# Optimization experiments

Measured on AMD Instinct MI355X. Metric: run time of the kernel, lower is better.

## Reference

```python
import jax, jax.numpy as jnp
import numpy as np

HID, NH, HD, KTS = 512, 8, 64, 4
BATCH, SEQ = 2, 1024
CLIP, AMIN, AMAX = 2.0, 1e-4, 0.9995
ROPE_BASE = 10000.0


def _rmsnorm(x, w, eps=1e-5):
    rms = jnp.sqrt(jnp.mean(x * x, axis=-1, keepdims=True) + eps)
    return x / rms * w


def _rope(q, k, base=ROPE_BASE):
    # q,k: [B,T,H,D], D even -> rotate-half formulation (split halves, not interleaved)
    T, D = q.shape[1], q.shape[-1]
    half = D // 2
    pos = jnp.arange(T, dtype=q.dtype)
    inv_freq = 1.0 / (base ** (jnp.arange(half, dtype=q.dtype) / half))
    ang = pos[:, None] * inv_freq[None, :]            # [T, half]
    cos = jnp.cos(ang)[None, :, None, :]
    sin = jnp.sin(ang)[None, :, None, :]
    def rot(x):
        x1, x2 = x[..., :half], x[..., half:]
        return jnp.concatenate([x1 * cos - x2 * sin, x1 * sin + x2 * cos], axis=-1)
    return rot(q), rot(k)


def setup_inputs() -> dict:
    key = jax.random.key(0)
    ks = jax.random.split(key, 10)
    def xavier(k, shape):
        lim = float(np.sqrt(6.0 / (shape[0] + shape[1])))
        return jax.random.uniform(k, shape, jnp.float32, -lim, lim)
    x = jax.random.normal(ks[0], (BATCH, SEQ, HID), jnp.float32)
    mask = jnp.ones((BATCH, SEQ), jnp.int32)
    qW = xavier(ks[1], (HID, HID))
    kW = xavier(ks[2], (HID, HID))
    vW = xavier(ks[3], (HID, HID))
    oW = xavier(ks[4], (HID, HID))
    ob = jnp.zeros((HID,), jnp.float32)
    # alpha bias from geometric half-lives [32,128,512,2048]
    half_lives = np.array([32.0 * (4.0 ** i) for i in range(KTS)], dtype=np.float64)
    alphas = np.clip(np.exp(-np.log(2.0) / half_lives), AMIN, AMAX)
    alphas = np.tile(alphas, NH)
    ab = jnp.asarray(np.log(alphas / (1.0 - alphas)), jnp.float32)
    aW = 0.01 * jax.random.normal(ks[5], (NH * KTS, HID), jnp.float32)
    mW = 0.01 * jax.random.normal(ks[6], (NH * KTS, HID), jnp.float32)
    mb = jnp.zeros((NH * KTS,), jnp.float32)
    in_w = jnp.ones((HID,), jnp.float32)
    kn_w = jnp.ones((HD,), jnp.float32)
    vn_w = jnp.ones((HD,), jnp.float32)
    ln_w = jnp.ones((HID,), jnp.float32)
    ln_b = jnp.zeros((HID,), jnp.float32)
    return dict(x=x, in_w=in_w, qW=qW, kW=kW, vW=vW, aW=aW, ab=ab, mW=mW, mb=mb,
                oW=oW, ob=ob, kn_w=kn_w, vn_w=vn_w, ln_w=ln_w, ln_b=ln_b, mask=mask)


def reference(x, in_w, qW, kW, vW, aW, ab, mW, mb, oW, ob, kn_w, vn_w, ln_w, ln_b, mask):
    B, T, _ = x.shape
    xn = _rmsnorm(x, in_w)
    q = (xn @ qW.T).reshape(B, T, NH, HD)
    k = (xn @ kW.T).reshape(B, T, NH, HD)
    v = (xn @ vW.T).reshape(B, T, NH, HD)
    q, k = _rope(q, k)
    k = _rmsnorm(k, kn_w)
    v = _rmsnorm(v, vn_w)
    alpha = jnp.clip(jax.nn.sigmoid(xn @ aW.T + ab), AMIN, AMAX).reshape(B, T, NH, KTS)
    mix = jax.nn.softmax((xn @ mW.T + mb).reshape(B, T, NH, KTS), axis=-1)
    m = mask.astype(jnp.float32)
    c = float(np.sqrt(HD)) * CLIP

    def step(h, inp):
        # h: [B,H,K,D,D] fp32 state; delta-rule write + multi-timescale decay + norm clip
        q_t, k_t, v_t, a_t, mx_t, m_t = inp
        outer = (k_t * m_t[:, None, None])[:, :, None, :, None] * v_t[:, :, None, None, :]
        h = h * a_t[..., None, None] + outer
        norm = jnp.sqrt(jnp.sum(h * h, axis=(-2, -1), keepdims=True))
        h = h * jnp.minimum(c / (norm + 1e-6), 1.0)
        y = jnp.einsum('bhd,bhkde->bhke', q_t, h)
        return h, jnp.einsum('bhk,bhkd->bhd', mx_t, y)

    h0 = jnp.zeros((B, NH, KTS, HD, HD), jnp.float32)
    tm = lambda a: jnp.moveaxis(a, 1, 0)  # time-major
    xs = (tm(q), tm(k), tm(v), tm(alpha), tm(mix), m.T)
    _, ys = jax.lax.scan(jax.checkpoint(step), h0, xs)  # ys: [T,B,H,D]
    y = jnp.moveaxis(ys, 0, 1).reshape(B, T, HID)
    out = y @ oW.T + ob  # dropout p=0 (eval)
    r = x + out
    mu = jnp.mean(r, axis=-1, keepdims=True)
    var = jnp.mean((r - mu) ** 2, axis=-1, keepdims=True)
    return (r - mu) / jnp.sqrt(var + 1e-5) * ln_w + ln_b
```

## Files before the change

### kernel.cpp

```cpp
#include <hip/hip_runtime.h>
#include <math.h>

#define SEQT 1024
#define NTOK 2048
#define HIDN 512
#define NHD 8
#define HDIM 64
#define KTSN 4

__device__ __forceinline__ float wred(float v) {
#pragma unroll
  for (int off = 32; off; off >>= 1) v += __shfl_xor(v, off, 64);
  return v;
}

template <int CTRL>
__device__ __forceinline__ float rra(float v) {
  return v + __int_as_float(__builtin_amdgcn_update_dpp(
                 0, __float_as_int(v), CTRL, 0xf, 0xf, true));
}
__device__ __forceinline__ float rlane(float v, int l) {
  return __int_as_float(__builtin_amdgcn_readlane(__float_as_int(v), l));
}
__device__ __forceinline__ float wsum64_fast(float v) {
  v = rra<0x121>(v);
  v = rra<0x122>(v);
  v = rra<0x124>(v);
  v = rra<0x128>(v);
  return (rlane(v, 0) + rlane(v, 16)) + (rlane(v, 32) + rlane(v, 48));
}

__global__ __launch_bounds__(256) void k_rmsnorm_in(
    const float* __restrict__ x, const float* __restrict__ w, float* __restrict__ xn) {
  int m = blockIdx.x;
  int tid = threadIdx.x;
  const float* row = x + (size_t)m * HIDN;
  float2 v = *(const float2*)(row + tid * 2);
  float ss = wred(v.x * v.x + v.y * v.y);
  __shared__ float red[4];
  int lane = tid & 63, wv = tid >> 6;
  if (lane == 0) red[wv] = ss;
  __syncthreads();
  float tot = red[0] + red[1] + red[2] + red[3];
  float inv = rsqrtf(tot * (1.0f / HIDN) + 1e-5f);
  float2 wv2 = *(const float2*)(w + tid * 2);
  float2 o;
  o.x = v.x * inv * wv2.x;
  o.y = v.y * inv * wv2.y;
  *(float2*)(xn + (size_t)m * HIDN + tid * 2) = o;
}

__global__ __launch_bounds__(256) void k_gemm_qkv(
    const float* __restrict__ A, const float* __restrict__ Bq,
    const float* __restrict__ Bk, const float* __restrict__ Bv,
    float* __restrict__ Cq, float* __restrict__ Ck, float* __restrict__ Cv) {
  __shared__ __align__(16) float As[32][68];
  __shared__ __align__(16) float Bs0[32][68];
  __shared__ __align__(16) float Bs1[32][68];
  __shared__ __align__(16) float Bs2[32][68];
  int tid = threadIdx.x;
  int m0 = blockIdx.x * 64, n0 = blockIdx.y * 64;
  int tm = tid >> 4, tn = tid & 15;
  float aq[4][4] = {}, ak[4][4] = {}, av4[4][4] = {};
  int rr = tid >> 2, cc = (tid & 3) * 8;
  for (int k0 = 0; k0 < HIDN; k0 += 32) {
    const float* s0 = A + (size_t)(m0 + rr) * HIDN + k0 + cc;
    float4 a0 = *(const float4*)s0;
    float4 a1 = *(const float4*)(s0 + 4);
    As[cc + 0][rr] = a0.x; As[cc + 1][rr] = a0.y; As[cc + 2][rr] = a0.z; As[cc + 3][rr] = a0.w;
    As[cc + 4][rr] = a1.x; As[cc + 5][rr] = a1.y; As[cc + 6][rr] = a1.z; As[cc + 7][rr] = a1.w;
    size_t boff = (size_t)(n0 + rr) * HIDN + k0 + cc;
    float4 b0 = *(const float4*)(Bq + boff);
    float4 b1 = *(const float4*)(Bq + boff + 4);
    Bs0[cc + 0][rr] = b0.x; Bs0[cc + 1][rr] = b0.y; Bs0[cc + 2][rr] = b0.z; Bs0[cc + 3][rr] = b0.w;
    Bs0[cc + 4][rr] = b1.x; Bs0[cc + 5][rr] = b1.y; Bs0[cc + 6][rr] = b1.z; Bs0[cc + 7][rr] = b1.w;
    b0 = *(const float4*)(Bk + boff);
    b1 = *(const float4*)(Bk + boff + 4);
    Bs1[cc + 0][rr] = b0.x; Bs1[cc + 1][rr] = b0.y; Bs1[cc + 2][rr] = b0.z; Bs1[cc + 3][rr] = b0.w;
    Bs1[cc + 4][rr] = b1.x; Bs1[cc + 5][rr] = b1.y; Bs1[cc + 6][rr] = b1.z; Bs1[cc + 7][rr] = b1.w;
    b0 = *(const float4*)(Bv + boff);
    b1 = *(const float4*)(Bv + boff + 4);
    Bs2[cc + 0][rr] = b0.x; Bs2[cc + 1][rr] = b0.y; Bs2[cc + 2][rr] = b0.z; Bs2[cc + 3][rr] = b0.w;
    Bs2[cc + 4][rr] = b1.x; Bs2[cc + 5][rr] = b1.y; Bs2[cc + 6][rr] = b1.z; Bs2[cc + 7][rr] = b1.w;
    __syncthreads();
#pragma unroll
    for (int kk = 0; kk < 32; ++kk) {
      float4 a4 = *(const float4*)&As[kk][tm * 4];
      float4 q4 = *(const float4*)&Bs0[kk][tn * 4];
      float4 k4 = *(const float4*)&Bs1[kk][tn * 4];
      float4 v4 = *(const float4*)&Bs2[kk][tn * 4];
      float aa[4] = {a4.x, a4.y, a4.z, a4.w};
      float qq[4] = {q4.x, q4.y, q4.z, q4.w};
      float kk_[4] = {k4.x, k4.y, k4.z, k4.w};
      float vv[4] = {v4.x, v4.y, v4.z, v4.w};
#pragma unroll
      for (int i = 0; i < 4; ++i)
#pragma unroll
        for (int j = 0; j < 4; ++j) {
          aq[i][j] = fmaf(aa[i], qq[j], aq[i][j]);
          ak[i][j] = fmaf(aa[i], kk_[j], ak[i][j]);
          av4[i][j] = fmaf(aa[i], vv[j], av4[i][j]);
        }
    }
    __syncthreads();
  }
#pragma unroll
  for (int i = 0; i < 4; ++i) {
    size_t mr = (size_t)(m0 + tm * 4 + i) * HIDN;
#pragma unroll
    for (int j = 0; j < 4; ++j) {
      int nc = n0 + tn * 4 + j;
      Cq[mr + nc] = aq[i][j];
      Ck[mr + nc] = ak[i][j];
      Cv[mr + nc] = av4[i][j];
    }
  }
}

__global__ __launch_bounds__(256) void k_gemm_am(
    const float* __restrict__ A, const float* __restrict__ Ba,
    const float* __restrict__ Bm, float* __restrict__ Ca, float* __restrict__ Cm) {
  __shared__ __align__(16) float As[32][68];
  __shared__ __align__(16) float Bs[32][68];
  int tid = threadIdx.x;
  int m0 = blockIdx.x * 64;
  int tm = tid >> 4, tn = tid & 15;
  float acc[4][4] = {};
  int rr = tid >> 2, cc = (tid & 3) * 8;
  for (int k0 = 0; k0 < HIDN; k0 += 32) {
    const float* s0 = A + (size_t)(m0 + rr) * HIDN + k0 + cc;
    float4 a0 = *(const float4*)s0;
    float4 a1 = *(const float4*)(s0 + 4);
    As[cc + 0][rr] = a0.x; As[cc + 1][rr] = a0.y; As[cc + 2][rr] = a0.z; As[cc + 3][rr] = a0.w;
    As[cc + 4][rr] = a1.x; As[cc + 5][rr] = a1.y; As[cc + 6][rr] = a1.z; As[cc + 7][rr] = a1.w;
    const float* s1 = ((rr < 32) ? (Ba + (size_t)rr * HIDN) : (Bm + (size_t)(rr - 32) * HIDN)) + k0 + cc;
    float4 b0 = *(const float4*)s1;
    float4 b1 = *(const float4*)(s1 + 4);
    Bs[cc + 0][rr] = b0.x; Bs[cc + 1][rr] = b0.y; Bs[cc + 2][rr] = b0.z; Bs[cc + 3][rr] = b0.w;
    Bs[cc + 4][rr] = b1.x; Bs[cc + 5][rr] = b1.y; Bs[cc + 6][rr] = b1.z; Bs[cc + 7][rr] = b1.w;
    __syncthreads();
#pragma unroll
    for (int kk = 0; kk < 32; ++kk) {
      float4 a4 = *(const float4*)&As[kk][tm * 4];
      float4 b4 = *(const float4*)&Bs[kk][tn * 4];
      float aa[4] = {a4.x, a4.y, a4.z, a4.w};
      float bb[4] = {b4.x, b4.y, b4.z, b4.w};
#pragma unroll
      for (int i = 0; i < 4; ++i)
#pragma unroll
        for (int j = 0; j < 4; ++j) acc[i][j] = fmaf(aa[i], bb[j], acc[i][j]);
    }
    __syncthreads();
  }
#pragma unroll
  for (int i = 0; i < 4; ++i) {
    int mr = m0 + tm * 4 + i;
#pragma unroll
    for (int j = 0; j < 4; ++j) {
      int nc = tn * 4 + j;
      if (nc < 32)
        Ca[(size_t)mr * 32 + nc] = acc[i][j];
      else
        Cm[(size_t)mr * 32 + nc - 32] = acc[i][j];
    }
  }
}

__global__ __launch_bounds__(256) void k_rope_table(float2* __restrict__ tab) {
  int idx = blockIdx.x * 256 + threadIdx.x;
  int t = idx >> 5, j = idx & 31;
  float invf = (float)exp2(-(double)j * (13.287712379549449 / 32.0));
  float ang = (float)t * invf;
  double s, c;
  sincos((double)ang, &s, &c);
  tab[idx] = make_float2((float)c, (float)s);
}

__global__ __launch_bounds__(256) void k_postproc(
    const float* __restrict__ q_in, const float* __restrict__ k_in, const float* __restrict__ v_in,
    const float* __restrict__ a_pre, const float* __restrict__ m_pre,
    const float* __restrict__ ab, const float* __restrict__ mb,
    const float* __restrict__ kn_w, const float* __restrict__ vn_w,
    const float2* __restrict__ tab,
    float* __restrict__ qh, float* __restrict__ kh, float* __restrict__ vh,
    float* __restrict__ av, float* __restrict__ mv) {
  int wid = blockIdx.x * 4 + (threadIdx.x >> 6);
  int lane = threadIdx.x & 63;
  int b = wid >> 13;
  int rem = wid & 8191;
  int t = rem >> 3;
  int h = rem & 7;
  size_t src = (size_t)(b * SEQT + t) * HIDN + h * HDIM + lane;
  float qv = q_in[src], kv = k_in[src], vv = v_in[src];
  float2 cs = tab[t * 32 + (lane & 31)];
  float qpart = __shfl_xor(qv, 32, 64);
  float kpart = __shfl_xor(kv, 32, 64);
  float qr = (lane < 32) ? (qv * cs.x - qpart * cs.y) : (qpart * cs.y + qv * cs.x);
  float kr = (lane < 32) ? (kv * cs.x - kpart * cs.y) : (kpart * cs.y + kv * cs.x);
  float kss = wred(kr * kr);
  float kn = kr * rsqrtf(kss * (1.0f / HDIM) + 1e-5f) * kn_w[lane];
  float vss = wred(vv * vv);
  float vn = vv * rsqrtf(vss * (1.0f / HDIM) + 1e-5f) * vn_w[lane];
  size_t dst = ((size_t)(b * NHD + h) * SEQT + t) * HDIM + lane;
  qh[dst] = qr;
  kh[dst] = kn;
  vh[dst] = vn;
  if (lane < 4) {
    int col = h * 4 + lane;
    float pa = a_pre[(size_t)(b * SEQT + t) * 32 + col] + ab[col];
    float al = 1.0f / (1.0f + expf(-pa));
    al = fminf(fmaxf(al, 1e-4f), 0.9995f);
    float pm = m_pre[(size_t)(b * SEQT + t) * 32 + col] + mb[col];
    float mx = pm;
    mx = fmaxf(mx, __shfl_xor(mx, 1, 64));
    mx = fmaxf(mx, __shfl_xor(mx, 2, 64));
    float e = expf(pm - mx);
    float sum = e;
    sum += __shfl_xor(sum, 1, 64);
    sum += __shfl_xor(sum, 2, 64);
    size_t adst = ((size_t)(b * NHD + h) * KTSN + lane) * SEQT + t;
    av[adst] = al;
    mv[adst] = e / sum;
  }
}

#define G16P(X) \
  X(0, 0) X(1, 1) X(2, 2) X(3, 3) X(4, 0) X(5, 1) X(6, 2) X(7, 3) \
  X(8, 0) X(9, 1) X(10, 2) X(11, 3) X(12, 0) X(13, 1) X(14, 2) X(15, 3)

#define DECLH(g, a) float h##g = 0.f;

#define UPDH(g, a)                                \
  {                                               \
    float ks = rlane(kqs0, g);                    \
    h##g = fmaf(h##g, ag, ks * vem);              \
    sq##a = fmaf(h##g, h##g, sq##a);              \
  }

#define YUPH(g, a)                                \
  {                                               \
    float qs = rlane(kqs0, 16 + (g));             \
    y##a = fmaf(qs, h##g, y##a);                  \
  }

__global__ __launch_bounds__(256, 1) void k_scan(
    const float* __restrict__ qh, const float* __restrict__ kh, const float* __restrict__ vh,
    const float* __restrict__ av, const float* __restrict__ mv, const int* __restrict__ mask,
    float* __restrict__ y0p, float* __restrict__ y1p, float* __restrict__ y2p,
    float* __restrict__ y3p) {
  int c = blockIdx.x;
  int kt = c & 3;
  int bh = c >> 2;
  int b = bh >> 3;
  int h = bh & 7;
  int tid = threadIdx.x;
  int w = tid >> 6;
  int lane = tid & 63;
  int dbase = w * 16;

  const float* kp = kh + (size_t)bh * SEQT * HDIM;
  const float* qp = qh + (size_t)bh * SEQT * HDIM;
  const float* vp = vh + (size_t)bh * SEQT * HDIM;
  const float* ap = av + (size_t)c * SEQT;
  const float* mp = mv + (size_t)c * SEQT;
  const int* mk = mask + (size_t)b * SEQT;
  float* ysel = (kt == 0) ? y0p : (kt == 1) ? y1p : (kt == 2) ? y2p : y3p;
  float* ypo = ysel + (size_t)(b * SEQT) * HIDN + h * HDIM + lane;

  __shared__ __align__(16) float sqb[2][4];
  __shared__ __align__(16) float ypart[2][4][64];
  __shared__ int cnt;

  G16P(DECLH)
  float gprev = 1.0f;

  int off = lane & 15;
  const float* kqbase = ((lane >> 4) & 1) ? qp : kp;
  int kqidx = dbase + off;

  float kqs0 = kqbase[kqidx];
  float kqs1 = kqbase[(size_t)1 * HDIM + kqidx];
  float kqs2 = kqbase[(size_t)2 * HDIM + kqidx];
  float vC = vp[lane], vD = vp[HDIM + lane], vE = vp[2 * HDIM + lane];
  float aC = ap[0], aD = ap[1], aE = ap[2];
  float mxC = mp[0], mxD = mp[1], mxE = mp[2];
  float mC = (float)mk[0], mD = (float)mk[1], mE = (float)mk[2];

  if (tid == 0) cnt = 0;
  __syncthreads();

  for (int t = 0; t < SEQT; ++t) {
    int t3 = t + 3;
    if (t3 > SEQT - 1) t3 = SEQT - 1;
    float kqN = kqbase[(size_t)t3 * HDIM + kqidx];
    float vN = vp[(size_t)t3 * HDIM + lane];
    float aN = ap[t3];
    float mxN = mp[t3];
    float mN = (float)mk[t3];

    float ag = aC * gprev;
    float vem = vC * mC;
    float sq0 = 0.f, sq1 = 0.f, sq2 = 0.f, sq3 = 0.f;
    G16P(UPDH)
    float sqw = wsum64_fast((sq0 + sq1) + (sq2 + sq3));
    int P = t & 1;
    if (lane == 0) sqb[P][w] = sqw;
    float y0 = 0.f, y1 = 0.f, y2 = 0.f, y3 = 0.f;
    G16P(YUPH)
    ypart[P][w][lane] = (y0 + y1) + (y2 + y3);
    asm volatile("s_waitcnt lgkmcnt(0)" ::: "memory");
    if (lane == 0) atomicAdd(&cnt, 1);
    {
      int target = 4 * (t + 1);
      while (*(volatile int*)&cnt < target) {
      }
    }
    asm volatile("" ::: "memory");
    float4 sq4 = *(const float4*)&sqb[P][0];
    float sqt = (sq4.x + sq4.y) + (sq4.z + sq4.w);
    float g = fminf(16.0f * rsqrtf(sqt), 1.0f);
    if (w == 0) {
      float ys = (ypart[P][0][lane] + ypart[P][1][lane]) +
                 (ypart[P][2][lane] + ypart[P][3][lane]);
      ypo[(size_t)t * HIDN] = (mxC * g) * ys;
    }
    gprev = g;

    kqs0 = kqs1; kqs1 = kqs2; kqs2 = kqN;
    vC = vD; vD = vE; vE = vN;
    aC = aD; aD = aE; aE = aN;
    mxC = mxD; mxD = mxE; mxE = mxN;
    mC = mD; mD = mE; mE = mN;
  }
}

__global__ __launch_bounds__(256) void k_gemm_out(
    const float* __restrict__ y0, const float* __restrict__ y1,
    const float* __restrict__ y2, const float* __restrict__ y3,
    const float* __restrict__ oW, const float* __restrict__ ob,
    const float* __restrict__ x, float* __restrict__ r) {
  __shared__ __align__(16) float As[32][68];
  __shared__ __align__(16) float Bs[32][68];
  int tid = threadIdx.x;
  int m0 = blockIdx.x * 64, n0 = blockIdx.y * 64;
  int tm = tid >> 4, tn = tid & 15;
  float acc[4][4] = {};
  int rr = tid >> 2, cc = (tid & 3) * 8;
  for (int k0 = 0; k0 < HIDN; k0 += 32) {
    size_t aoff = (size_t)(m0 + rr) * HIDN + k0 + cc;
#pragma unroll
    for (int half = 0; half < 2; ++half) {
      size_t sh = aoff + half * 4;
      float4 p0 = *(const float4*)(y0 + sh);
      float4 p1 = *(const float4*)(y1 + sh);
      float4 p2 = *(const float4*)(y2 + sh);
      float4 p3 = *(const float4*)(y3 + sh);
      int cbase = cc + half * 4;
      As[cbase + 0][rr] = p0.x + p1.x + p2.x + p3.x;
      As[cbase + 1][rr] = p0.y + p1.y + p2.y + p3.y;
      As[cbase + 2][rr] = p0.z + p1.z + p2.z + p3.z;
      As[cbase + 3][rr] = p0.w + p1.w + p2.w + p3.w;
    }
    const float* s1 = oW + (size_t)(n0 + rr) * HIDN + k0 + cc;
    float4 b0 = *(const float4*)s1;
    float4 b1 = *(const float4*)(s1 + 4);
    Bs[cc + 0][rr] = b0.x; Bs[cc + 1][rr] = b0.y; Bs[cc + 2][rr] = b0.z; Bs[cc + 3][rr] = b0.w;
    Bs[cc + 4][rr] = b1.x; Bs[cc + 5][rr] = b1.y; Bs[cc + 6][rr] = b1.z; Bs[cc + 7][rr] = b1.w;
    __syncthreads();
#pragma unroll
    for (int kk = 0; kk < 32; ++kk) {
      float4 a4 = *(const float4*)&As[kk][tm * 4];
      float4 b4 = *(const float4*)&Bs[kk][tn * 4];
      float aa[4] = {a4.x, a4.y, a4.z, a4.w};
      float bb[4] = {b4.x, b4.y, b4.z, b4.w};
#pragma unroll
      for (int i = 0; i < 4; ++i)
#pragma unroll
        for (int j = 0; j < 4; ++j) acc[i][j] += aa[i] * bb[j];
    }
    __syncthreads();
  }
#pragma unroll
  for (int i = 0; i < 4; ++i) {
    int mr = m0 + tm * 4 + i;
#pragma unroll
    for (int j = 0; j < 4; ++j) {
      int nc = n0 + tn * 4 + j;
      r[(size_t)mr * HIDN + nc] = x[(size_t)mr * HIDN + nc] + acc[i][j] + ob[nc];
    }
  }
}

__global__ __launch_bounds__(256) void k_layernorm(
    const float* __restrict__ r, const float* __restrict__ w, const float* __restrict__ bb,
    float* __restrict__ out) {
  int m = blockIdx.x;
  int tid = threadIdx.x;
  const float* row = r + (size_t)m * HIDN;
  float2 v = *(const float2*)(row + tid * 2);
  float s = wred(v.x + v.y);
  float ss = wred(v.x * v.x + v.y * v.y);
  __shared__ float r1[4], r2[4];
  int lane = tid & 63, wv = tid >> 6;
  if (lane == 0) {
    r1[wv] = s;
    r2[wv] = ss;
  }
  __syncthreads();
  float S = r1[0] + r1[1] + r1[2] + r1[3];
  float SS = r2[0] + r2[1] + r2[2] + r2[3];
  float mu = S * (1.0f / HIDN);
  float var = SS * (1.0f / HIDN) - mu * mu;
  float inv = rsqrtf(var + 1e-5f);
  float2 w2 = *(const float2*)(w + tid * 2);
  float2 b2 = *(const float2*)(bb + tid * 2);
  float2 o;
  o.x = (v.x - mu) * inv * w2.x + b2.x;
  o.y = (v.y - mu) * inv * w2.y + b2.y;
  *(float2*)(out + (size_t)m * HIDN + tid * 2) = o;
}

extern "C" void kernel_launch(void* const* d_in, const int* in_sizes, int n_in,
                              void* d_out, int out_size, void* d_ws, size_t ws_size,
                              hipStream_t stream) {
  const float* x = (const float*)d_in[0];
  const float* in_w = (const float*)d_in[1];
  const float* qW = (const float*)d_in[2];
  const float* kW = (const float*)d_in[3];
  const float* vW = (const float*)d_in[4];
  const float* aW = (const float*)d_in[5];
  const float* ab = (const float*)d_in[6];
  const float* mW = (const float*)d_in[7];
  const float* mb = (const float*)d_in[8];
  const float* oW = (const float*)d_in[9];
  const float* ob = (const float*)d_in[10];
  const float* kn_w = (const float*)d_in[11];
  const float* vn_w = (const float*)d_in[12];
  const float* ln_w = (const float*)d_in[13];
  const float* ln_b = (const float*)d_in[14];
  const int* mask = (const int*)d_in[15];

  float* ws = (float*)d_ws;
  float* xn = ws + 0;
  float* qb = ws + 1048576;
  float* kb = ws + 2097152;
  float* vb = ws + 3145728;
  float* apre = ws + 4194304;
  float* mpre = ws + 4259840;
  float2* tab = (float2*)(ws + 4325376);
  float* qh = ws + 4390912;
  float* kh = ws + 5439488;
  float* vh = ws + 6488064;
  float* avv = ws + 7536640;
  float* mvv = ws + 7602176;
  float* y3 = ws + 7667712;
  float* y0 = qb;
  float* y1 = kb;
  float* y2 = vb;
  float* rr = xn;

  k_rope_table<<<128, 256, 0, stream>>>(tab);
  k_rmsnorm_in<<<NTOK, 256, 0, stream>>>(x, in_w, xn);
  dim3 gBig(32, 8);
  k_gemm_qkv<<<gBig, 256, 0, stream>>>(xn, qW, kW, vW, qb, kb, vb);
  k_gemm_am<<<32, 256, 0, stream>>>(xn, aW, mW, apre, mpre);
  k_postproc<<<4096, 256, 0, stream>>>(qb, kb, vb, apre, mpre, ab, mb, kn_w, vn_w, tab,
                                       qh, kh, vh, avv, mvv);
  k_scan<<<64, 256, 0, stream>>>(qh, kh, vh, avv, mvv, mask, y0, y1, y2, y3);
  k_gemm_out<<<gBig, 256, 0, stream>>>(y0, y1, y2, y3, oW, ob, x, rr);
  k_layernorm<<<NTOK, 256, 0, stream>>>(rr, ln_w, ln_b, (float*)d_out);
  (void)in_sizes; (void)n_in; (void)out_size; (void)ws_size;
}
```

Before: 707.1 us.

## Scan two timesteps per barrier using algebraic norm and output recurrences

Rewrites the sequential delta-rule scan to process two timesteps per cross-wave barrier. The squared Frobenius norm and outputs are now obtained algebraically from the previous norm, h·k·v contractions and precomputed per-step scalars (q·k, |k|²|v|², adjacent-step k·k, v·v, q·k dot products). A new k_cross kernel and extra reductions in postproc produce those scalars. This halves the number of spin-barrier synchronisations on the serial critical path. In exchange it adds a kernel launch, reuses the xn workspace region for the scalar buffers, and may accumulate floating-point error in the recursive norm, which is clamped at zero.

```diff
diff --git a/kernel.cpp b/kernel.cpp
--- a/kernel.cpp
+++ b/kernel.cpp
@@ -183,7 +183,8 @@
     const float* __restrict__ kn_w, const float* __restrict__ vn_w,
     const float2* __restrict__ tab,
     float* __restrict__ qh, float* __restrict__ kh, float* __restrict__ vh,
-    float* __restrict__ av, float* __restrict__ mv) {
+    float* __restrict__ av, float* __restrict__ mv,
+    float* __restrict__ qkd, float* __restrict__ kvq) {
   int wid = blockIdx.x * 4 + (threadIdx.x >> 6);
   int lane = threadIdx.x & 63;
   int b = wid >> 13;
@@ -205,6 +206,14 @@
   qh[dst] = qr;
   kh[dst] = kn;
   vh[dst] = vn;
+  float knss = wred(kn * kn);
+  float vnss = wred(vn * vn);
+  float qkdot = wred(qr * kn);
+  if (lane == 0) {
+    size_t sdst = (size_t)(b * NHD + h) * SEQT + t;
+    qkd[sdst] = qkdot;
+    kvq[sdst] = knss * vnss;
+  }
   if (lane < 4) {
     int col = h * 4 + lane;
     float pa = a_pre[(size_t)(b * SEQT + t) * 32 + col] + ab[col];
@@ -224,28 +233,54 @@
   }
 }
 
+__global__ __launch_bounds__(256) void k_cross(
+    const float* __restrict__ qh, const float* __restrict__ kh, const float* __restrict__ vh,
+    float* __restrict__ kkx, float* __restrict__ vvx, float* __restrict__ qxx) {
+  int wid = blockIdx.x * 4 + (threadIdx.x >> 6);
+  int lane = threadIdx.x & 63;
+  int bh = wid >> 10;
+  int t = wid & 1023;
+  size_t sidx = (size_t)bh * SEQT + t;
+  if (t == 0) {
+    if (lane == 0) { kkx[sidx] = 0.f; vvx[sidx] = 0.f; qxx[sidx] = 0.f; }
+    return;
+  }
+  size_t base = (size_t)bh * SEQT * HDIM;
+  float kc = kh[base + (size_t)t * HDIM + lane];
+  float kp = kh[base + (size_t)(t - 1) * HDIM + lane];
+  float vc = vh[base + (size_t)t * HDIM + lane];
+  float vpv = vh[base + (size_t)(t - 1) * HDIM + lane];
+  float qc = qh[base + (size_t)t * HDIM + lane];
+  float s1 = wred(kc * kp);
+  float s2 = wred(vc * vpv);
+  float s3 = wred(qc * kp);
+  if (lane == 0) { kkx[sidx] = s1; vvx[sidx] = s2; qxx[sidx] = s3; }
+}
+
 #define G16P(X) \
   X(0, 0) X(1, 1) X(2, 2) X(3, 3) X(4, 0) X(5, 1) X(6, 2) X(7, 3) \
   X(8, 0) X(9, 1) X(10, 2) X(11, 3) X(12, 0) X(13, 1) X(14, 2) X(15, 3)
 
 #define DECLH(g, a) float h##g = 0.f;
-
-#define UPDH(g, a)                                \
-  {                                               \
-    float ks = rlane(kqs0, g);                    \
-    h##g = fmaf(h##g, ag, ks * vem);              \
-    sq##a = fmaf(h##g, h##g, sq##a);              \
-  }
-
-#define YUPH(g, a)                                \
-  {                                               \
-    float qs = rlane(kqs0, 16 + (g));             \
-    y##a = fmaf(qs, h##g, y##a);                  \
+#define HUP0(g, a) h##g = fmaf(h##g, ag0, rlane(kqj0, (g)) * vm0);
+#define HUP1(g, a) h##g = fmaf(h##g, ag1, rlane(kqj1, (g)) * vm1);
+#define MV4(g, a)                                   \
+  {                                                 \
+    float k2_ = rlane(kqj2, (g));                   \
+    float q2_ = rlane(kqj2, 16 + (g));              \
+    float k3_ = rlane(kqj3, (g));                   \
+    float q3_ = rlane(kqj3, 16 + (g));              \
+    zk2##a = fmaf(k2_, h##g, zk2##a);               \
+    zk3##a = fmaf(k3_, h##g, zk3##a);               \
+    pv2##a = fmaf(q2_, h##g, pv2##a);               \
+    pv3##a = fmaf(q3_, h##g, pv3##a);               \
   }
 
 __global__ __launch_bounds__(256, 1) void k_scan(
     const float* __restrict__ qh, const float* __restrict__ kh, const float* __restrict__ vh,
     const float* __restrict__ av, const float* __restrict__ mv, const int* __restrict__ mask,
+    const float* __restrict__ qkd, const float* __restrict__ kvq,
+    const float* __restrict__ kkx, const float* __restrict__ vvx, const float* __restrict__ qxx,
     float* __restrict__ y0p, float* __restrict__ y1p, float* __restrict__ y2p,
     float* __restrict__ y3p) {
   int c = blockIdx.x;
@@ -263,74 +298,134 @@
   const float* vp = vh + (size_t)bh * SEQT * HDIM;
   const float* ap = av + (size_t)c * SEQT;
   const float* mp = mv + (size_t)c * SEQT;
+  const float* qkp = qkd + (size_t)bh * SEQT;
+  const float* kvp = kvq + (size_t)bh * SEQT;
+  const float* kkp = kkx + (size_t)bh * SEQT;
+  const float* vvp = vvx + (size_t)bh * SEQT;
+  const float* qxp = qxx + (size_t)bh * SEQT;
   const int* mk = mask + (size_t)b * SEQT;
   float* ysel = (kt == 0) ? y0p : (kt == 1) ? y1p : (kt == 2) ? y2p : y3p;
   float* ypo = ysel + (size_t)(b * SEQT) * HIDN + h * HDIM + lane;
 
-  __shared__ __align__(16) float sqb[2][4];
-  __shared__ __align__(16) float ypart[2][4][64];
+  __shared__ __align__(16) float2 Zb[2][4];
+  __shared__ __align__(16) float Pb[2][2][4][64];
   __shared__ int cnt;
 
   G16P(DECLH)
   float gprev = 1.0f;
+  float usq = 0.0f;
 
   int off = lane & 15;
   const float* kqbase = ((lane >> 4) & 1) ? qp : kp;
   int kqidx = dbase + off;
 
-  float kqs0 = kqbase[kqidx];
-  float kqs1 = kqbase[(size_t)1 * HDIM + kqidx];
-  float kqs2 = kqbase[(size_t)2 * HDIM + kqidx];
-  float vC = vp[lane], vD = vp[HDIM + lane], vE = vp[2 * HDIM + lane];
-  float aC = ap[0], aD = ap[1], aE = ap[2];
-  float mxC = mp[0], mxD = mp[1], mxE = mp[2];
-  float mC = (float)mk[0], mD = (float)mk[1], mE = (float)mk[2];
+  float kqj0 = kqbase[kqidx];
+  float kqj1 = kqbase[(size_t)1 * HDIM + kqidx];
+  float kqj2 = kqbase[(size_t)2 * HDIM + kqidx];
+  float kqj3 = kqbase[(size_t)3 * HDIM + kqidx];
+  float kqj4 = kqbase[(size_t)4 * HDIM + kqidx];
+  float kqj5 = kqbase[(size_t)5 * HDIM + kqidx];
+  float vj0 = vp[lane], vj1 = vp[HDIM + lane], vj2 = vp[2 * HDIM + lane];
+  float vj3 = vp[3 * HDIM + lane], vj4 = vp[4 * HDIM + lane], vj5 = vp[5 * HDIM + lane];
+  float a0 = ap[0], a1 = ap[1], a2 = ap[2], a3 = ap[3], a4 = ap[4], a5 = ap[5];
+  float mx0 = mp[0], mx1 = mp[1], mx2 = mp[2], mx3 = mp[3], mx4 = mp[4], mx5 = mp[5];
+  float m0 = (float)mk[0], m1 = (float)mk[1], m2 = (float)mk[2];
+  float m3 = (float)mk[3], m4 = (float)mk[4], m5 = (float)mk[5];
+  float qk0 = qkp[0], qk1 = qkp[1], qk2 = qkp[2], qk3 = qkp[3], qk4 = qkp[4], qk5 = qkp[5];
+  float kv0 = kvp[0], kv1 = kvp[1], kv2 = kvp[2], kv3 = kvp[3], kv4 = kvp[4], kv5 = kvp[5];
+  float kko0 = kkp[1], kko1 = kkp[3], kko2 = kkp[5];
+  float vvo0 = vvp[1], vvo1 = vvp[3], vvo2 = vvp[5];
+  float qxo0 = qxp[1], qxo1 = qxp[3], qxo2 = qxp[5];
 
   if (tid == 0) cnt = 0;
+  if (lane == 0) Zb[0][w] = make_float2(0.f, 0.f);
+  Pb[0][0][w][lane] = 0.f;
+  Pb[0][1][w][lane] = 0.f;
   __syncthreads();
 
-  for (int t = 0; t < SEQT; ++t) {
-    int t3 = t + 3;
-    if (t3 > SEQT - 1) t3 = SEQT - 1;
-    float kqN = kqbase[(size_t)t3 * HDIM + kqidx];
-    float vN = vp[(size_t)t3 * HDIM + lane];
-    float aN = ap[t3];
-    float mxN = mp[t3];
-    float mN = (float)mk[t3];
-
-    float ag = aC * gprev;
-    float vem = vC * mC;
-    float sq0 = 0.f, sq1 = 0.f, sq2 = 0.f, sq3 = 0.f;
-    G16P(UPDH)
-    float sqw = wsum64_fast((sq0 + sq1) + (sq2 + sq3));
-    int P = t & 1;
-    if (lane == 0) sqb[P][w] = sqw;
-    float y0 = 0.f, y1 = 0.f, y2 = 0.f, y3 = 0.f;
-    G16P(YUPH)
-    ypart[P][w][lane] = (y0 + y1) + (y2 + y3);
+  for (int s = 0; s < SEQT; s += 2) {
+    int r = s >> 1;
+    int P = r & 1;
+    int t6 = s + 6, t7 = s + 7;
+    if (t6 > SEQT - 1) t6 = SEQT - 1;
+    if (t7 > SEQT - 1) t7 = SEQT - 1;
+    float kqN6 = kqbase[(size_t)t6 * HDIM + kqidx];
+    float kqN7 = kqbase[(size_t)t7 * HDIM + kqidx];
+    float vN6 = vp[(size_t)t6 * HDIM + lane];
+    float vN7 = vp[(size_t)t7 * HDIM + lane];
+    float aN6 = ap[t6], aN7 = ap[t7];
+    float mxN6 = mp[t6], mxN7 = mp[t7];
+    float mN6 = (float)mk[t6], mN7 = (float)mk[t7];
+    float qkN6 = qkp[t6], qkN7 = qkp[t7];
+    float kvN6 = kvp[t6], kvN7 = kvp[t7];
+    float kkN = kkp[t7], vvN = vvp[t7], qxN = qxp[t7];
+
+    float2 zb0 = Zb[P][0], zb1 = Zb[P][1], zb2 = Zb[P][2], zb3 = Zb[P][3];
+    float zs = (zb0.x + zb1.x) + (zb2.x + zb3.x);
+    float w1 = (zb0.y + zb1.y) + (zb2.y + zb3.y);
+
+    float ag0 = a0 * gprev;
+    float vm0 = m0 * vj0;
+    G16P(HUP0)
+    float usq0 = fmaf(ag0 * ag0, usq, fmaf(2.0f * ag0 * m0, zs, (m0 * m0) * kv0));
+    usq0 = fmaxf(usq0, 0.0f);
+    float g0 = fminf(16.0f * rsqrtf(usq0), 1.0f);
+
+    float z1 = fmaf(ag0, w1, (m0 * kko0) * vvo0);
+    float ag1 = a1 * g0;
+    float vm1 = m1 * vj1;
+    G16P(HUP1)
+    float usq1 = fmaf(ag1 * ag1, usq0, fmaf(2.0f * ag1 * m1, z1, (m1 * m1) * kv1));
+    usq1 = fmaxf(usq1, 0.0f);
+    float g1 = fminf(16.0f * rsqrtf(usq1), 1.0f);
+
+    float zk20 = 0.f, zk21 = 0.f, zk22 = 0.f, zk23 = 0.f;
+    float zk30 = 0.f, zk31 = 0.f, zk32 = 0.f, zk33 = 0.f;
+    float pv20 = 0.f, pv21 = 0.f, pv22 = 0.f, pv23 = 0.f;
+    float pv30 = 0.f, pv31 = 0.f, pv32 = 0.f, pv33 = 0.f;
+    G16P(MV4)
+    float zk2s = (zk20 + zk21) + (zk22 + zk23);
+    float zk3s = (zk30 + zk31) + (zk32 + zk33);
+    float Z0n = wsum64_fast(zk2s * vj2);
+    float Z1n = wsum64_fast(zk3s * vj3);
+    float P0n = (pv20 + pv21) + (pv22 + pv23);
+    float P1n = (pv30 + pv31) + (pv32 + pv33);
+
+    if (w == 0) {
+      float pe = (Pb[P][0][0][lane] + Pb[P][0][1][lane]) +
+                 (Pb[P][0][2][lane] + Pb[P][0][3][lane]);
+      ypo[(size_t)s * HIDN] = (g0 * mx0) * fmaf(ag0, pe, (m0 * qk0) * vj0);
+    } else if (w == 1) {
+      float pe = (Pb[P][1][0][lane] + Pb[P][1][1][lane]) +
+                 (Pb[P][1][2][lane] + Pb[P][1][3][lane]);
+      float p1 = fmaf(ag0, pe, (m0 * qxo0) * vj0);
+      ypo[(size_t)(s + 1) * HIDN] = (g1 * mx1) * fmaf(ag1, p1, (m1 * qk1) * vj1);
+    }
+
+    if (lane == 0) Zb[P ^ 1][w] = make_float2(Z0n, Z1n);
+    Pb[P ^ 1][0][w][lane] = P0n;
+    Pb[P ^ 1][1][w][lane] = P1n;
     asm volatile("s_waitcnt lgkmcnt(0)" ::: "memory");
     if (lane == 0) atomicAdd(&cnt, 1);
     {
-      int target = 4 * (t + 1);
+      int target = 4 * (r + 1);
       while (*(volatile int*)&cnt < target) {
       }
     }
     asm volatile("" ::: "memory");
-    float4 sq4 = *(const float4*)&sqb[P][0];
-    float sqt = (sq4.x + sq4.y) + (sq4.z + sq4.w);
-    float g = fminf(16.0f * rsqrtf(sqt), 1.0f);
-    if (w == 0) {
-      float ys = (ypart[P][0][lane] + ypart[P][1][lane]) +
-                 (ypart[P][2][lane] + ypart[P][3][lane]);
-      ypo[(size_t)t * HIDN] = (mxC * g) * ys;
-    }
-    gprev = g;
-
-    kqs0 = kqs1; kqs1 = kqs2; kqs2 = kqN;
-    vC = vD; vD = vE; vE = vN;
-    aC = aD; aD = aE; aE = aN;
-    mxC = mxD; mxD = mxE; mxE = mxN;
-    mC = mD; mD = mE; mE = mN;
+
+    gprev = g1;
+    usq = usq1;
+    kqj0 = kqj2; kqj1 = kqj3; kqj2 = kqj4; kqj3 = kqj5; kqj4 = kqN6; kqj5 = kqN7;
+    vj0 = vj2; vj1 = vj3; vj2 = vj4; vj3 = vj5; vj4 = vN6; vj5 = vN7;
+    a0 = a2; a1 = a3; a2 = a4; a3 = a5; a4 = aN6; a5 = aN7;
+    mx0 = mx2; mx1 = mx3; mx2 = mx4; mx3 = mx5; mx4 = mxN6; mx5 = mxN7;
+    m0 = m2; m1 = m3; m2 = m4; m3 = m5; m4 = mN6; m5 = mN7;
+    qk0 = qk2; qk1 = qk3; qk2 = qk4; qk3 = qk5; qk4 = qkN6; qk5 = qkN7;
+    kv0 = kv2; kv1 = kv3; kv2 = kv4; kv3 = kv5; kv4 = kvN6; kv5 = kvN7;
+    kko0 = kko1; kko1 = kko2; kko2 = kkN;
+    vvo0 = vvo1; vvo1 = vvo2; vvo2 = vvN;
+    qxo0 = qxo1; qxo1 = qxo2; qxo2 = qxN;
   }
 }
 
@@ -458,6 +553,11 @@
   float* y1 = kb;
   float* y2 = vb;
   float* rr = xn;
+  float* qkd = ws + 0;
+  float* kvq = ws + 16384;
+  float* kkx = ws + 32768;
+  float* vvx = ws + 49152;
+  float* qxx = ws + 65536;
 
   k_rope_table<<<128, 256, 0, stream>>>(tab);
   k_rmsnorm_in<<<NTOK, 256, 0, stream>>>(x, in_w, xn);
@@ -465,8 +565,10 @@
   k_gemm_qkv<<<gBig, 256, 0, stream>>>(xn, qW, kW, vW, qb, kb, vb);
   k_gemm_am<<<32, 256, 0, stream>>>(xn, aW, mW, apre, mpre);
   k_postproc<<<4096, 256, 0, stream>>>(qb, kb, vb, apre, mpre, ab, mb, kn_w, vn_w, tab,
-                                       qh, kh, vh, avv, mvv);
-  k_scan<<<64, 256, 0, stream>>>(qh, kh, vh, avv, mvv, mask, y0, y1, y2, y3);
+                                       qh, kh, vh, avv, mvv, qkd, kvq);
+  k_cross<<<4096, 256, 0, stream>>>(qh, kh, vh, kkx, vvx, qxx);
+  k_scan<<<64, 256, 0, stream>>>(qh, kh, vh, avv, mvv, mask, qkd, kvq, kkx, vvx, qxx,
+                                 y0, y1, y2, y3);
   k_gemm_out<<<gBig, 256, 0, stream>>>(y0, y1, y2, y3, oW, ob, x, rr);
   k_layernorm<<<NTOK, 256, 0, stream>>>(rr, ln_w, ln_b, (float*)d_out);
   (void)in_sizes; (void)n_in; (void)out_size; (void)ws_size;
```

New measurement: 702.0 us (median of 2 runs). About the same (-0.7%).
